# Kernel tuning notes

Measured on AMD Instinct MI355X. Metric: run time of the kernel, lower is better.

Reference implementation:

```python
import jax, jax.numpy as jnp
import numpy as np

NUM_EMBEDDINGS = 512
EMBEDDING_DIM = 128
COMMITMENT_COST = 0.25
DECAY = 0.99
EPSILON = 1e-5


def setup_inputs() -> dict:
    key = jax.random.key(0)
    k1, k2 = jax.random.split(key)
    inputs = jax.random.normal(k1, (2, EMBEDDING_DIM, 32, 32, 32), dtype=jnp.float32)
    embedding_w = jax.random.normal(k2, (NUM_EMBEDDINGS, EMBEDDING_DIM), dtype=jnp.float32)
    ema_cluster_size = jnp.zeros((NUM_EMBEDDINGS,), dtype=jnp.float32)
    ema_w = embedding_w  # buffer initialized as a clone of the codebook
    return {"inputs": inputs, "embedding_w": embedding_w,
            "ema_cluster_size": ema_cluster_size, "ema_w": ema_w}


def reference(inputs, embedding_w, ema_cluster_size, ema_w):
    B, C, D, H, W = inputs.shape
    K = embedding_w.shape[0]

    # flatten: channel-last then [N, C]
    flat_input = jnp.transpose(inputs, (0, 2, 3, 4, 1)).reshape(-1, C)  # [N, C]
    N = flat_input.shape[0]

    # squared-euclidean distances to the codebook: [N, K]
    distances = ((flat_input ** 2).sum(axis=1, keepdims=True)
                 + (embedding_w ** 2).sum(axis=1)[None, :]
                 - 2.0 * flat_input @ embedding_w.T)

    encoding_indices = jnp.argmax(-distances, axis=1)  # [N] int32

    # entropy regularizer over soft assignments (temperature 1.0)
    probs = jax.nn.softmax(-distances, axis=1)
    entropy_loss = 0.01 * (-jnp.sum(probs * jnp.log(probs + 1e-8)) / N)

    # embed: gather codebook rows, reshape to channel-first volume
    quantized_raw = embedding_w[encoding_indices].reshape(B, D, H, W, C)
    quantized_raw = jnp.transpose(quantized_raw, (0, 4, 1, 2, 3))  # [B, C, D, H, W]

    # commitment loss (codebook is EMA-updated, not grad-updated)
    commit_loss = COMMITMENT_COST * jnp.mean(
        (jax.lax.stop_gradient(quantized_raw) - inputs) ** 2)
    loss = commit_loss + entropy_loss

    # straight-through estimator output
    quantized = inputs + jax.lax.stop_gradient(quantized_raw - inputs)

    # EMA codebook update (scatter-add over argmin clusters)
    encodings_sum = jnp.zeros((K,), flat_input.dtype).at[encoding_indices].add(1.0)
    dw = jnp.zeros((K, C), flat_input.dtype).at[encoding_indices].add(flat_input)
    new_cluster_size = DECAY * ema_cluster_size + (1.0 - DECAY) * encodings_sum
    n_total = new_cluster_size.sum()
    smoothed = (new_cluster_size + EPSILON) / (n_total + K * EPSILON) * n_total
    new_ema_w = DECAY * ema_w + (1.0 - DECAY) * dw
    new_embedding_w = new_ema_w / smoothed[:, None]

    encoding_indices_vol = encoding_indices.reshape(B, D, H, W)
    return (quantized, loss, encoding_indices_vol,
            new_cluster_size, new_ema_w, new_embedding_w)
```

## Files before the change

kernel.cpp:

```cpp
#include <hip/hip_runtime.h>

#define LOSS_OFF  8388608
#define IDX_OFF   8388609
#define NCS_OFF   8454145
#define EMAW_OFF  8454657
#define EMB_OFF   8520193

typedef __attribute__((ext_vector_type(8))) short short8;
typedef __attribute__((ext_vector_type(4))) float f32x4;

__device__ __forceinline__ unsigned short bf16r(float x) {
  unsigned u = __float_as_uint(x);
  u += 0x7fff + ((u >> 16) & 1);
  return (unsigned short)(u >> 16);
}
__device__ __forceinline__ float bf16tof(unsigned short h) {
  return __uint_as_float(((unsigned)h) << 16);
}

__global__ __launch_bounds__(256) void prep_kernel(const float* __restrict__ emb,
    unsigned short* __restrict__ ehig, unsigned short* __restrict__ elog,
    float* __restrict__ eeg)
{
  __shared__ float r1[256];
  const int t = threadIdx.x;
  const int k = blockIdx.x * 2 + (t >> 7);
  const int c = t & 127;
  float x = emb[k * 128 + c];
  unsigned short hh = bf16r(x);
  ehig[k * 128 + c] = hh;
  elog[k * 128 + c] = bf16r(x - bf16tof(hh));
  r1[t] = x * x;
  __syncthreads();
  #pragma unroll
  for (int off = 64; off; off >>= 1) {
    if ((t & 127) < off) r1[t] += r1[t + off];
    __syncthreads();
  }
  if ((t & 127) == 0) eeg[k] = r1[t];
}

__global__ __attribute__((amdgpu_flat_work_group_size(256, 256),
                          amdgpu_waves_per_eu(2, 4)))
void dist_kernel(const float* __restrict__ inputs, const float* __restrict__ emb,
                 const unsigned short* __restrict__ ehig,
                 const unsigned short* __restrict__ elog,
                 const float* __restrict__ eeg, float* __restrict__ out,
                 float* __restrict__ idxws, float* __restrict__ sums)
{
  __shared__ __align__(16) unsigned short esm[2][64 * 136];
  __shared__ float eeL[512];
  __shared__ float xxs[128];
  __shared__ int   ibkL[128];
  __shared__ float red[8];
  float* xs = (float*)&esm[0][0];

  const int t = threadIdx.x, lane = t & 63, wave = t >> 6;
  const int n0 = blockIdx.x * 128;
  const int b = n0 >> 15, s0 = n0 & 32767;
  const int col = lane & 15, quad = lane >> 4;

  eeL[t] = eeg[t]; eeL[256 + t] = eeg[256 + t];

  short8 ahi[2][4], alo[2][4];
  for (int r4 = 0; r4 < 4; ++r4) {
    __syncthreads();
    {
      const int rr = t & 31, c0 = (t >> 5) * 16;
      const float* src = inputs + (size_t)b * 128 * 32768 + s0 + r4 * 32 + rr;
      #pragma unroll
      for (int i = 0; i < 16; ++i)
        xs[rr * 132 + c0 + i] = src[(size_t)(c0 + i) * 32768];
    }
    __syncthreads();
    if (wave == r4) {
      #pragma unroll
      for (int rg = 0; rg < 2; ++rg) {
        float xacc = 0.f;
        const float* xr = &xs[(rg * 16 + col) * 132 + quad * 8];
        #pragma unroll
        for (int q = 0; q < 4; ++q) {
          float v[8];
          *(float4*)&v[0] = *(const float4*)(xr + q * 32);
          *(float4*)&v[4] = *(const float4*)(xr + q * 32 + 4);
          short8 h8, l8;
          #pragma unroll
          for (int j = 0; j < 8; ++j) {
            unsigned short hh = bf16r(v[j]);
            h8[j] = (short)hh;
            l8[j] = (short)bf16r(v[j] - bf16tof(hh));
            xacc += v[j] * v[j];
          }
          ahi[rg][q] = h8; alo[rg][q] = l8;
        }
        xacc += __shfl_xor(xacc, 16);
        xacc += __shfl_xor(xacc, 32);
        if (lane < 16) xxs[wave * 32 + rg * 16 + lane] = xacc;
      }
    }
  }

  float mS[8], sS[8], tS[8]; int kS[8];
  #pragma unroll
  for (int i = 0; i < 8; ++i) { mS[i] = 1e30f; sS[i] = 0.f; tS[i] = 0.f; kS[i] = 0; }

  for (int st = 0; st < 8; ++st) {
    __syncthreads();
    {
      const int k = t >> 2, cB = (t & 3) * 32;
      const size_t go = (size_t)(st * 64 + k) * 128 + cB;
      const uint4* gh = (const uint4*)(ehig + go);
      const uint4* gl = (const uint4*)(elog + go);
      uint4* dh = (uint4*)&esm[0][k * 136 + cB];
      uint4* dl = (uint4*)&esm[1][k * 136 + cB];
      #pragma unroll
      for (int i = 0; i < 4; ++i) dh[i] = gh[i];
      #pragma unroll
      for (int i = 0; i < 4; ++i) dl[i] = gl[i];
    }
    __syncthreads();
    for (int kt = 0; kt < 4; ++kt) {
      f32x4 ac0 = {0.f, 0.f, 0.f, 0.f}, ac1 = {0.f, 0.f, 0.f, 0.f};
      const int boff = (kt * 16 + col) * 136 + quad * 8;
      #pragma unroll
      for (int q = 0; q < 4; ++q) {
        short8 bh = *(const short8*)&esm[0][boff + q * 32];
        short8 bl = *(const short8*)&esm[1][boff + q * 32];
        ac0 = __builtin_amdgcn_mfma_f32_16x16x32_bf16(alo[0][q], bh, ac0, 0, 0, 0);
        ac1 = __builtin_amdgcn_mfma_f32_16x16x32_bf16(alo[1][q], bh, ac1, 0, 0, 0);
        ac0 = __builtin_amdgcn_mfma_f32_16x16x32_bf16(ahi[0][q], bl, ac0, 0, 0, 0);
        ac1 = __builtin_amdgcn_mfma_f32_16x16x32_bf16(ahi[1][q], bl, ac1, 0, 0, 0);
        ac0 = __builtin_amdgcn_mfma_f32_16x16x32_bf16(ahi[0][q], bh, ac0, 0, 0, 0);
        ac1 = __builtin_amdgcn_mfma_f32_16x16x32_bf16(ahi[1][q], bh, ac1, 0, 0, 0);
      }
      const int code = st * 64 + kt * 16 + col;
      const float eec = eeL[code];
      #pragma unroll
      for (int si = 0; si < 8; ++si) {
        float a = (si < 4) ? ac0[si & 3] : ac1[si & 3];
        float d = eec - 2.f * a;
        float mo = mS[si];
        float mn = fminf(mo, d);
        float E  = __expf(mn - fmaxf(mo, d));
        bool nw  = d < mo;
        float f  = nw ? E : 1.f;
        float e2 = nw ? 1.f : E;
        tS[si] = (tS[si] + (mn - mo) * sS[si]) * f + (mn - d) * e2;
        sS[si] = sS[si] * f + e2;
        kS[si] = nw ? code : kS[si];
        mS[si] = mn;
      }
    }
  }

  #pragma unroll
  for (int off = 1; off <= 8; off <<= 1) {
    #pragma unroll
    for (int si = 0; si < 8; ++si) {
      float m2 = __shfl_xor(mS[si], off);
      float S2 = __shfl_xor(sS[si], off);
      float T2 = __shfl_xor(tS[si], off);
      int   k2 = __shfl_xor(kS[si], off);
      float mo = mS[si];
      float mn = fminf(mo, m2);
      float f1 = __expf(mn - mo);
      float f2 = __expf(mn - m2);
      tS[si] = (tS[si] + (mn - mo) * sS[si]) * f1 + (T2 + (mn - m2) * S2) * f2;
      sS[si] = sS[si] * f1 + S2 * f2;
      if (m2 < mo || (m2 == mo && k2 < kS[si])) kS[si] = k2;
      mS[si] = mn;
    }
  }

  float cacc = 0.f, eacc = 0.f;
  #pragma unroll
  for (int si = 0; si < 8; ++si) {
    int rg = si >> 2, reg = si & 3;
    int row = wave * 32 + rg * 16 + quad * 4 + reg;
    if (col == 0) {
      float xx = xxs[row];
      int rn = n0 + row;
      float fk = (float)kS[si];
      out[IDX_OFF + rn] = fk;
      idxws[rn] = fk;
      ibkL[row] = kS[si];
      cacc += xx + mS[si];
      eacc += tS[si] / sS[si] - __logf(sS[si]);
    }
  }
  cacc += __shfl_xor(cacc, 16); cacc += __shfl_xor(cacc, 32);
  eacc += __shfl_xor(eacc, 16); eacc += __shfl_xor(eacc, 32);
  if (lane == 0) { red[wave] = cacc; red[4 + wave] = eacc; }
  __syncthreads();
  if (t == 0) {
    unsafeAtomicAdd(&sums[0], red[0] + red[1] + red[2] + red[3]);
    unsafeAtomicAdd(&sums[1], red[4] + red[5] + red[6] + red[7]);
  }

  for (int r4 = 0; r4 < 4; ++r4) {
    __syncthreads();
    {
      const int rr = t & 31, c0 = (t >> 5) * 16;
      const int kq = ibkL[r4 * 32 + rr];
      const float* src = emb + (size_t)kq * 128 + c0;
      float4 v0 = *(const float4*)(src);
      float4 v1 = *(const float4*)(src + 4);
      float4 v2 = *(const float4*)(src + 8);
      float4 v3 = *(const float4*)(src + 12);
      float* dst = &xs[rr * 132 + c0];
      *(float4*)dst = v0; *(float4*)(dst + 4) = v1;
      *(float4*)(dst + 8) = v2; *(float4*)(dst + 12) = v3;
    }
    __syncthreads();
    {
      const int l7 = t & 7;
      #pragma unroll
      for (int pp = 0; pp < 4; ++pp) {
        int c = (t >> 3) + 32 * pp;
        float4 v;
        v.x = xs[(4 * l7 + 0) * 132 + c];
        v.y = xs[(4 * l7 + 1) * 132 + c];
        v.z = xs[(4 * l7 + 2) * 132 + c];
        v.w = xs[(4 * l7 + 3) * 132 + c];
        *(float4*)(out + ((size_t)b * 128 + c) * 32768 + s0 + r4 * 32 + 4 * l7) = v;
      }
    }
  }
}

__global__ __launch_bounds__(256) void scatter_kernel(
    const float* __restrict__ inputs, const float* __restrict__ idxws,
    float* __restrict__ partial, float* __restrict__ cpart, int S)
{
  __shared__ float acc[512 * 9];
  __shared__ float cnts[512];
  const int t = threadIdx.x;
  const int s = blockIdx.x >> 4, ccB = blockIdx.x & 15;
  const int R = 65536 / S;
  for (int m = t; m < 512 * 9; m += 256) acc[m] = 0.f;
  if (ccB == 0) for (int m = t; m < 512; m += 256) cnts[m] = 0.f;
  __syncthreads();
  const int l = t & 63, cg = t >> 6;
  for (int it = 0; it < R / 256; ++it) {
    int n = s * R + it * 256;
    int bb = n >> 15;
    int sp = (n & 32767) + 4 * l;
    float4 i4 = *(const float4*)(idxws + n + 4 * l);
    int k0 = (int)i4.x, k1 = (int)i4.y, k2 = (int)i4.z, k3 = (int)i4.w;
    #pragma unroll
    for (int ci = 0; ci < 2; ++ci) {
      int c = cg * 2 + ci;
      float4 x4 = *(const float4*)(inputs + ((size_t)bb * 128 + ccB * 8 + c) * 32768 + sp);
      atomicAdd(&acc[k0 * 9 + c], x4.x);
      atomicAdd(&acc[k1 * 9 + c], x4.y);
      atomicAdd(&acc[k2 * 9 + c], x4.z);
      atomicAdd(&acc[k3 * 9 + c], x4.w);
    }
    if (ccB == 0 && cg == 0) {
      atomicAdd(&cnts[k0], 1.f); atomicAdd(&cnts[k1], 1.f);
      atomicAdd(&cnts[k2], 1.f); atomicAdd(&cnts[k3], 1.f);
    }
  }
  __syncthreads();
  for (int m = t; m < 512 * 8; m += 256) {
    int k = m >> 3, c = m & 7;
    partial[(size_t)s * 65536 + k * 128 + ccB * 8 + c] = acc[k * 9 + c];
  }
  if (ccB == 0) for (int m = t; m < 512; m += 256) cpart[s * 512 + m] = cnts[m];
}

__global__ __launch_bounds__(512) void c1_kernel(const float* __restrict__ ecs,
    const float* __restrict__ cpart, const float* __restrict__ sums,
    float* __restrict__ invs, float* __restrict__ out, int S)
{
  __shared__ float sred[512];
  int t = threadIdx.x;
  float cnt = 0.f;
  for (int s = 0; s < S; ++s) cnt += cpart[s * 512 + t];
  float cn = 0.99f * ecs[t] + 0.01f * cnt;
  out[NCS_OFF + t] = cn;
  sred[t] = cn;
  __syncthreads();
  for (int o = 256; o; o >>= 1) {
    if (t < o) sred[t] += sred[t + o];
    __syncthreads();
  }
  float ntot = sred[0];
  float sm = (cn + 1e-5f) / (ntot + 0.00512f) * ntot;
  invs[t] = 1.f / sm;
  if (t == 0)
    out[LOSS_OFF] = 0.25f * sums[0] / 8388608.f - 0.01f * sums[1] / 65536.f;
}

__global__ __launch_bounds__(256) void c2_kernel(const float* __restrict__ emaw,
    const float* __restrict__ partial, const float* __restrict__ invs,
    float* __restrict__ out, int S)
{
  int i = blockIdx.x * 256 + threadIdx.x;
  float dwv = 0.f;
  for (int s = 0; s < S; ++s) dwv += partial[(size_t)s * 65536 + i];
  float val = 0.99f * emaw[i] + 0.01f * dwv;
  out[EMAW_OFF + i] = val;
  out[EMB_OFF + i] = val * invs[i >> 7];
}

extern "C" void kernel_launch(void* const* d_in, const int* in_sizes, int n_in,
                              void* d_out, int out_size, void* d_ws, size_t ws_size,
                              hipStream_t stream) {
  const float* inputs = (const float*)d_in[0];
  const float* emb    = (const float*)d_in[1];
  const float* ecs    = (const float*)d_in[2];
  const float* emaw   = (const float*)d_in[3];
  float* out = (float*)d_out;
  float* wsf = (float*)d_ws;
  (void)in_sizes; (void)n_in; (void)out_size;

  size_t wsfl = ws_size / 4;
  int S = 32;
  while (S > 1 && (size_t)S * 66048 + 132128 > wsfl) S >>= 1;

  float* partial = wsf;
  float* cpart   = partial + (size_t)S * 65536;
  float* idxws   = cpart + (size_t)S * 512;
  float* sums    = idxws + 65536;
  float* eeg     = sums + 16;
  float* invs    = eeg + 512;
  unsigned short* ehig = (unsigned short*)(invs + 512);
  unsigned short* elog = ehig + 65536;

  hipMemsetAsync(sums, 0, 16 * sizeof(float), stream);
  prep_kernel   <<<256,    256, 0, stream>>>(emb, ehig, elog, eeg);
  dist_kernel   <<<512,    256, 0, stream>>>(inputs, emb, ehig, elog, eeg, out, idxws, sums);
  scatter_kernel<<<16 * S, 256, 0, stream>>>(inputs, idxws, partial, cpart, S);
  c1_kernel     <<<1,      512, 0, stream>>>(ecs, cpart, sums, invs, out, S);
  c2_kernel     <<<256,    256, 0, stream>>>(emaw, partial, invs, out, S);
}
```

Before: 213.8 us.

## Fuse codebook prep into distance kernel with double-buffered tiles; merge finalize kernels

```diff
diff --git a/kernel.cpp b/kernel.cpp
--- a/kernel.cpp
+++ b/kernel.cpp
@@ -18,59 +18,34 @@
   return __uint_as_float(((unsigned)h) << 16);
 }
 
-__global__ __launch_bounds__(256) void prep_kernel(const float* __restrict__ emb,
-    unsigned short* __restrict__ ehig, unsigned short* __restrict__ elog,
-    float* __restrict__ eeg)
-{
-  __shared__ float r1[256];
-  const int t = threadIdx.x;
-  const int k = blockIdx.x * 2 + (t >> 7);
-  const int c = t & 127;
-  float x = emb[k * 128 + c];
-  unsigned short hh = bf16r(x);
-  ehig[k * 128 + c] = hh;
-  elog[k * 128 + c] = bf16r(x - bf16tof(hh));
-  r1[t] = x * x;
-  __syncthreads();
-  #pragma unroll
-  for (int off = 64; off; off >>= 1) {
-    if ((t & 127) < off) r1[t] += r1[t + off];
-    __syncthreads();
-  }
-  if ((t & 127) == 0) eeg[k] = r1[t];
-}
-
 __global__ __attribute__((amdgpu_flat_work_group_size(256, 256),
                           amdgpu_waves_per_eu(2, 4)))
 void dist_kernel(const float* __restrict__ inputs, const float* __restrict__ emb,
-                 const unsigned short* __restrict__ ehig,
-                 const unsigned short* __restrict__ elog,
-                 const float* __restrict__ eeg, float* __restrict__ out,
-                 float* __restrict__ idxws, float* __restrict__ sums)
+                 float* __restrict__ out, float* __restrict__ idxws,
+                 float* __restrict__ sums)
 {
-  __shared__ __align__(16) unsigned short esm[2][64 * 136];
-  __shared__ float eeL[512];
+  __shared__ __align__(16) short esm[2][2][32 * 136];
+  __shared__ float eeS[2][32];
   __shared__ float xxs[128];
   __shared__ int   ibkL[128];
   __shared__ float red[8];
-  float* xs = (float*)&esm[0][0];
+  float* xs = (float*)&esm[0][0][0];
 
   const int t = threadIdx.x, lane = t & 63, wave = t >> 6;
   const int n0 = blockIdx.x * 128;
   const int b = n0 >> 15, s0 = n0 & 32767;
   const int col = lane & 15, quad = lane >> 4;
-
-  eeL[t] = eeg[t]; eeL[256 + t] = eeg[256 + t];
+  const int kk = t >> 3, c0 = (t & 7) * 16;
 
   short8 ahi[2][4], alo[2][4];
   for (int r4 = 0; r4 < 4; ++r4) {
     __syncthreads();
     {
-      const int rr = t & 31, c0 = (t >> 5) * 16;
+      const int rr = t & 31, cc = (t >> 5) * 16;
       const float* src = inputs + (size_t)b * 128 * 32768 + s0 + r4 * 32 + rr;
       #pragma unroll
       for (int i = 0; i < 16; ++i)
-        xs[rr * 132 + c0 + i] = src[(size_t)(c0 + i) * 32768];
+        xs[rr * 132 + cc + i] = src[(size_t)(cc + i) * 32768];
     }
     __syncthreads();
     if (wave == r4) {
@@ -99,33 +74,54 @@
       }
     }
   }
+  __syncthreads();
 
   float mS[8], sS[8], tS[8]; int kS[8];
   #pragma unroll
   for (int i = 0; i < 8; ++i) { mS[i] = 1e30f; sS[i] = 0.f; tS[i] = 0.f; kS[i] = 0; }
 
-  for (int st = 0; st < 8; ++st) {
-    __syncthreads();
-    {
-      const int k = t >> 2, cB = (t & 3) * 32;
-      const size_t go = (size_t)(st * 64 + k) * 128 + cB;
-      const uint4* gh = (const uint4*)(ehig + go);
-      const uint4* gl = (const uint4*)(elog + go);
-      uint4* dh = (uint4*)&esm[0][k * 136 + cB];
-      uint4* dl = (uint4*)&esm[1][k * 136 + cB];
-      #pragma unroll
-      for (int i = 0; i < 4; ++i) dh[i] = gh[i];
-      #pragma unroll
-      for (int i = 0; i < 4; ++i) dl[i] = gl[i];
-    }
-    __syncthreads();
-    for (int kt = 0; kt < 4; ++kt) {
+  float4 pf0, pf1, pf2, pf3;
+  {
+    const float* src = emb + (size_t)kk * 128 + c0;
+    pf0 = ((const float4*)src)[0]; pf1 = ((const float4*)src)[1];
+    pf2 = ((const float4*)src)[2]; pf3 = ((const float4*)src)[3];
+    float v[16];
+    *(float4*)&v[0] = pf0; *(float4*)&v[4] = pf1;
+    *(float4*)&v[8] = pf2; *(float4*)&v[12] = pf3;
+    short8 h0, h1, l0, l1; float sq = 0.f;
+    #pragma unroll
+    for (int j = 0; j < 8; ++j) {
+      unsigned short hh = bf16r(v[j]);
+      h0[j] = (short)hh; l0[j] = (short)bf16r(v[j] - bf16tof(hh));
+      sq += v[j] * v[j];
+      unsigned short hh2 = bf16r(v[8 + j]);
+      h1[j] = (short)hh2; l1[j] = (short)bf16r(v[8 + j] - bf16tof(hh2));
+      sq += v[8 + j] * v[8 + j];
+    }
+    *(short8*)&esm[0][0][kk * 136 + c0] = h0;
+    *(short8*)&esm[0][0][kk * 136 + c0 + 8] = h1;
+    *(short8*)&esm[0][1][kk * 136 + c0] = l0;
+    *(short8*)&esm[0][1][kk * 136 + c0 + 8] = l1;
+    sq += __shfl_xor(sq, 1); sq += __shfl_xor(sq, 2); sq += __shfl_xor(sq, 4);
+    if ((t & 7) == 0) eeS[0][kk] = sq;
+  }
+
+  for (int st = 0; st < 16; ++st) {
+    const int pb = st & 1;
+    if (st < 15) {
+      const float* src = emb + (size_t)((st + 1) * 32 + kk) * 128 + c0;
+      pf0 = ((const float4*)src)[0]; pf1 = ((const float4*)src)[1];
+      pf2 = ((const float4*)src)[2]; pf3 = ((const float4*)src)[3];
+    }
+    __syncthreads();
+    #pragma unroll
+    for (int kt = 0; kt < 2; ++kt) {
       f32x4 ac0 = {0.f, 0.f, 0.f, 0.f}, ac1 = {0.f, 0.f, 0.f, 0.f};
       const int boff = (kt * 16 + col) * 136 + quad * 8;
       #pragma unroll
       for (int q = 0; q < 4; ++q) {
-        short8 bh = *(const short8*)&esm[0][boff + q * 32];
-        short8 bl = *(const short8*)&esm[1][boff + q * 32];
+        short8 bh = *(const short8*)&esm[pb][0][boff + q * 32];
+        short8 bl = *(const short8*)&esm[pb][1][boff + q * 32];
         ac0 = __builtin_amdgcn_mfma_f32_16x16x32_bf16(alo[0][q], bh, ac0, 0, 0, 0);
         ac1 = __builtin_amdgcn_mfma_f32_16x16x32_bf16(alo[1][q], bh, ac1, 0, 0, 0);
         ac0 = __builtin_amdgcn_mfma_f32_16x16x32_bf16(ahi[0][q], bl, ac0, 0, 0, 0);
@@ -133,8 +129,8 @@
         ac0 = __builtin_amdgcn_mfma_f32_16x16x32_bf16(ahi[0][q], bh, ac0, 0, 0, 0);
         ac1 = __builtin_amdgcn_mfma_f32_16x16x32_bf16(ahi[1][q], bh, ac1, 0, 0, 0);
       }
-      const int code = st * 64 + kt * 16 + col;
-      const float eec = eeL[code];
+      const int code = st * 32 + kt * 16 + col;
+      const float eec = eeS[pb][kt * 16 + col];
       #pragma unroll
       for (int si = 0; si < 8; ++si) {
         float a = (si < 4) ? ac0[si & 3] : ac1[si & 3];
@@ -150,6 +146,28 @@
         kS[si] = nw ? code : kS[si];
         mS[si] = mn;
       }
+    }
+    if (st < 15) {
+      const int nb = pb ^ 1;
+      float v[16];
+      *(float4*)&v[0] = pf0; *(float4*)&v[4] = pf1;
+      *(float4*)&v[8] = pf2; *(float4*)&v[12] = pf3;
+      short8 h0, h1, l0, l1; float sq = 0.f;
+      #pragma unroll
+      for (int j = 0; j < 8; ++j) {
+        unsigned short hh = bf16r(v[j]);
+        h0[j] = (short)hh; l0[j] = (short)bf16r(v[j] - bf16tof(hh));
+        sq += v[j] * v[j];
+        unsigned short hh2 = bf16r(v[8 + j]);
+        h1[j] = (short)hh2; l1[j] = (short)bf16r(v[8 + j] - bf16tof(hh2));
+        sq += v[8 + j] * v[8 + j];
+      }
+      *(short8*)&esm[nb][0][kk * 136 + c0] = h0;
+      *(short8*)&esm[nb][0][kk * 136 + c0 + 8] = h1;
+      *(short8*)&esm[nb][1][kk * 136 + c0] = l0;
+      *(short8*)&esm[nb][1][kk * 136 + c0 + 8] = l1;
+      sq += __shfl_xor(sq, 1); sq += __shfl_xor(sq, 2); sq += __shfl_xor(sq, 4);
+      if ((t & 7) == 0) eeS[nb][kk] = sq;
     }
   }
 
@@ -200,14 +218,14 @@
   for (int r4 = 0; r4 < 4; ++r4) {
     __syncthreads();
     {
-      const int rr = t & 31, c0 = (t >> 5) * 16;
+      const int rr = t & 31, cc = (t >> 5) * 16;
       const int kq = ibkL[r4 * 32 + rr];
-      const float* src = emb + (size_t)kq * 128 + c0;
+      const float* src = emb + (size_t)kq * 128 + cc;
       float4 v0 = *(const float4*)(src);
       float4 v1 = *(const float4*)(src + 4);
       float4 v2 = *(const float4*)(src + 8);
       float4 v3 = *(const float4*)(src + 12);
-      float* dst = &xs[rr * 132 + c0];
+      float* dst = &xs[rr * 132 + cc];
       *(float4*)dst = v0; *(float4*)(dst + 4) = v1;
       *(float4*)(dst + 8) = v2; *(float4*)(dst + 12) = v3;
     }
@@ -269,39 +287,41 @@
   if (ccB == 0) for (int m = t; m < 512; m += 256) cpart[s * 512 + m] = cnts[m];
 }
 
-__global__ __launch_bounds__(512) void c1_kernel(const float* __restrict__ ecs,
+__global__ __launch_bounds__(256) void fin_kernel(const float* __restrict__ ecs,
+    const float* __restrict__ emaw, const float* __restrict__ partial,
     const float* __restrict__ cpart, const float* __restrict__ sums,
-    float* __restrict__ invs, float* __restrict__ out, int S)
-{
-  __shared__ float sred[512];
-  int t = threadIdx.x;
-  float cnt = 0.f;
-  for (int s = 0; s < S; ++s) cnt += cpart[s * 512 + t];
-  float cn = 0.99f * ecs[t] + 0.01f * cnt;
-  out[NCS_OFF + t] = cn;
-  sred[t] = cn;
-  __syncthreads();
-  for (int o = 256; o; o >>= 1) {
-    if (t < o) sred[t] += sred[t + o];
-    __syncthreads();
-  }
-  float ntot = sred[0];
-  float sm = (cn + 1e-5f) / (ntot + 0.00512f) * ntot;
-  invs[t] = 1.f / sm;
-  if (t == 0)
-    out[LOSS_OFF] = 0.25f * sums[0] / 8388608.f - 0.01f * sums[1] / 65536.f;
-}
-
-__global__ __launch_bounds__(256) void c2_kernel(const float* __restrict__ emaw,
-    const float* __restrict__ partial, const float* __restrict__ invs,
     float* __restrict__ out, int S)
 {
-  int i = blockIdx.x * 256 + threadIdx.x;
+  __shared__ float cn[512];
+  __shared__ float rsum[256];
+  const int t = threadIdx.x;
+  float local = 0.f;
+  for (int k = t; k < 512; k += 256) {
+    float c = 0.f;
+    for (int s = 0; s < S; ++s) c += cpart[s * 512 + k];
+    float v = 0.99f * ecs[k] + 0.01f * c;
+    cn[k] = v; local += v;
+  }
+  rsum[t] = local;
+  __syncthreads();
+  for (int o = 128; o; o >>= 1) {
+    if (t < o) rsum[t] += rsum[t + o];
+    __syncthreads();
+  }
+  const float ntot = rsum[0];
+  if (blockIdx.x == 0) {
+    for (int k = t; k < 512; k += 256) out[NCS_OFF + k] = cn[k];
+    if (t == 0)
+      out[LOSS_OFF] = 0.25f * sums[0] / 8388608.f - 0.01f * sums[1] / 65536.f;
+  }
+  const int i = blockIdx.x * 256 + t;
   float dwv = 0.f;
   for (int s = 0; s < S; ++s) dwv += partial[(size_t)s * 65536 + i];
   float val = 0.99f * emaw[i] + 0.01f * dwv;
+  const int k = i >> 7;
+  float sm = (cn[k] + 1e-5f) / (ntot + 0.00512f) * ntot;
   out[EMAW_OFF + i] = val;
-  out[EMB_OFF + i] = val * invs[i >> 7];
+  out[EMB_OFF + i] = val / sm;
 }
 
 extern "C" void kernel_launch(void* const* d_in, const int* in_sizes, int n_in,
@@ -316,22 +336,16 @@
   (void)in_sizes; (void)n_in; (void)out_size;
 
   size_t wsfl = ws_size / 4;
-  int S = 32;
-  while (S > 1 && (size_t)S * 66048 + 132128 > wsfl) S >>= 1;
+  int S = 16;
+  while (S > 1 && (size_t)S * 66048 + 65552 > wsfl) S >>= 1;
 
   float* partial = wsf;
   float* cpart   = partial + (size_t)S * 65536;
   float* idxws   = cpart + (size_t)S * 512;
   float* sums    = idxws + 65536;
-  float* eeg     = sums + 16;
-  float* invs    = eeg + 512;
-  unsigned short* ehig = (unsigned short*)(invs + 512);
-  unsigned short* elog = ehig + 65536;
 
   hipMemsetAsync(sums, 0, 16 * sizeof(float), stream);
-  prep_kernel   <<<256,    256, 0, stream>>>(emb, ehig, elog, eeg);
-  dist_kernel   <<<512,    256, 0, stream>>>(inputs, emb, ehig, elog, eeg, out, idxws, sums);
+  dist_kernel   <<<512,    256, 0, stream>>>(inputs, emb, out, idxws, sums);
   scatter_kernel<<<16 * S, 256, 0, stream>>>(inputs, idxws, partial, cpart, S);
-  c1_kernel     <<<1,      512, 0, stream>>>(ecs, cpart, sums, invs, out, S);
-  c2_kernel     <<<256,    256, 0, stream>>>(emaw, partial, invs, out, S);
-}
+  fin_kernel    <<<256,    256, 0, stream>>>(ecs, emaw, partial, cpart, sums, out, S);
+}
```

New measurement: 211.6 us. About the same (-1.0%).
